# Kernel optimization log

Measured on AMD Instinct MI355X. Metric: run time of the kernel, lower is better.

Reference implementation:

```python
import jax, jax.numpy as jnp
import numpy as np

B, T, IN, H, OUT, SIM = 256, 128, 128, 1024, 256, 4
EPS_BN = 1e-5
EPS_COS = 1e-8
NEG_SLOPE = 0.2


def setup_inputs() -> dict:
    key = jax.random.key(0)
    ks = jax.random.split(key, 12)
    rn = lambda k, s: jax.random.normal(k, s, dtype=jnp.float32) * 0.05
    return {
        "x": jax.random.normal(ks[0], (B, T, IN), dtype=jnp.float32),
        "W_emb": rn(ks[1], (H, IN)),
        "b_emb": jnp.zeros((H,), jnp.float32),
        "gamma": jnp.ones((H,), jnp.float32),
        "beta": jnp.zeros((H,), jnp.float32),
        "memory": jax.random.normal(ks[2], (1, T, H), dtype=jnp.float32),
        "w_ih_x": rn(ks[3], (3 * OUT, H)),
        "w_hh_x": rn(ks[4], (3 * OUT, OUT)),
        "b_ih_x": jnp.zeros((3 * OUT,), jnp.float32),
        "b_hh_x": jnp.zeros((3 * OUT,), jnp.float32),
        "w_ih_m": rn(ks[5], (3 * OUT, H)),
        "w_hh_m": rn(ks[6], (3 * OUT, OUT)),
        "b_ih_m": jnp.zeros((3 * OUT,), jnp.float32),
        "b_hh_m": jnp.zeros((3 * OUT,), jnp.float32),
        "W_sx": rn(ks[7], (SIM, OUT)),
        "b_sx": jnp.zeros((SIM,), jnp.float32),
        "W_sm": rn(ks[8], (SIM, OUT)),
        "b_sm": jnp.zeros((SIM,), jnp.float32),
    }


def _gru(x, h, w_ih, w_hh, b_ih, b_hh):
    # PyTorch GRUCell math
    gi = x @ w_ih.T + b_ih
    gh = h @ w_hh.T + b_hh
    i_r, i_z, i_n = jnp.split(gi, 3, axis=-1)
    h_r, h_z, h_n = jnp.split(gh, 3, axis=-1)
    r = jax.nn.sigmoid(i_r + h_r)
    z = jax.nn.sigmoid(i_z + h_z)
    n = jnp.tanh(i_n + r * h_n)
    return (1.0 - z) * n + z * h


def _forward(x, W_emb, b_emb, gamma, beta, memory,
             w_ih_x, w_hh_x, b_ih_x, b_hh_x,
             w_ih_m, w_hh_m, b_ih_m, b_hh_m,
             W_sx, b_sx, W_sm, b_sm):
    # embed + LeakyReLU(0.2)
    e = x @ W_emb.T + b_emb                                  # (B,T,H)
    e = jnp.where(e >= 0, e, NEG_SLOPE * e)
    # BatchNorm1d, training mode: per-channel stats over (B,T), biased var
    mean = jnp.mean(e, axis=(0, 1))
    var = jnp.mean((e - mean) ** 2, axis=(0, 1))
    e = (e - mean) * jax.lax.rsqrt(var + EPS_BN) * gamma + beta

    mem = memory[0]                                          # (T,H) shared across batch
    b = x.shape[0]

    def step(carry, inps):
        hx, hm = carry
        xt, mt = inps                                        # (B,H), (H,)
        mtb = jnp.broadcast_to(mt, (b, mt.shape[-1]))
        hx = _gru(xt, hx, w_ih_x, w_hh_x, b_ih_x, b_hh_x)    # (B,OUT)
        hm = _gru(mtb, hm, w_ih_m, w_hh_m, b_ih_m, b_hh_m)   # (B,OUT)
        # cosine-similarity addressing between sim_size projections
        qx = hx @ W_sx.T + b_sx                              # (B,SIM)
        qm = hm @ W_sm.T + b_sm
        num = jnp.sum(qx * qm, axis=-1)
        den = (jnp.maximum(jnp.linalg.norm(qx, axis=-1), EPS_COS)
               * jnp.maximum(jnp.linalg.norm(qm, axis=-1), EPS_COS))
        g = jax.nn.sigmoid(num / den)[:, None]               # gate in (0,1)
        out = g * hx + (1.0 - g) * hm
        return (hx, hm), out

    h0 = (jnp.zeros((b, OUT), e.dtype), jnp.zeros((b, OUT), e.dtype))
    (_, _), outs = jax.lax.scan(step, h0, (e.transpose(1, 0, 2), mem))
    return outs[-1].reshape(-1, OUT)                         # out of last timestep


def reference(x, W_emb, b_emb, gamma, beta, memory,
              w_ih_x, w_hh_x, b_ih_x, b_hh_x,
              w_ih_m, w_hh_m, b_ih_m, b_hh_m,
              W_sx, b_sx, W_sm, b_sm):
    return _forward(x, W_emb, b_emb, gamma, beta, memory,
                    w_ih_x, w_hh_x, b_ih_x, b_hh_x,
                    w_ih_m, w_hh_m, b_ih_m, b_hh_m,
                    W_sx, b_sx, W_sm, b_sm)
```

## Files before the change

kernel.cpp:

```cpp
#include <hip/hip_runtime.h>
#include <stdint.h>


typedef float  f32x4 __attribute__((ext_vector_type(4)));
typedef __bf16 bf16x8 __attribute__((ext_vector_type(8)));

#define B_   256
#define T_   128
#define IN_  128
#define H_   1024
#define OUT_ 256
#define M_   32768

static constexpr size_t OFF_XB    = 0;
static constexpr size_t OFF_WEMB  = 8388608;
static constexpr size_t OFF_WHX   = 8650752;
static constexpr size_t OFF_WHM   = 9043968;
static constexpr size_t OFF_SUM   = 9437184;
static constexpr size_t OFF_SSQ   = 9441280;
static constexpr size_t OFF_FLAGS = 9445376;
static constexpr size_t OFF_BIASX = 9453568;
static constexpr size_t OFF_GIM   = 9457664;
static constexpr size_t OFF_EACT  = 9654272;
static constexpr size_t OFF_GI    = 76763136;
static constexpr size_t OFF_HXF   = 127094784;
static constexpr size_t OFF_HMF   = 127356928;
static constexpr size_t OFF_WPX   = 127373312;

__device__ __forceinline__ float sigmoidf_(float x) {
    return __builtin_amdgcn_rcpf(1.0f + __expf(-x));
}
__device__ __forceinline__ float tanhf_(float x) {
    return 1.0f - 2.0f * __builtin_amdgcn_rcpf(1.0f + __expf(2.0f * x));
}
__device__ __forceinline__ float bf16bits_(unsigned short u) {
    return __uint_as_float(((unsigned)u) << 16);
}
__device__ __forceinline__ void gload_lds16(const void* g, void* l) {
    __builtin_amdgcn_global_load_lds(
        (const __attribute__((address_space(1))) unsigned int*)g,
        (__attribute__((address_space(3))) unsigned int*)l, 16, 0, 0);
}

__global__ void prep(const float* __restrict__ x, const float* __restrict__ wemb,
                     const float* __restrict__ whx, const float* __restrict__ whm,
                     __bf16* __restrict__ xb, __bf16* __restrict__ wembb,
                     __bf16* __restrict__ whxb, __bf16* __restrict__ whmb,
                     float* __restrict__ stats , int* __restrict__ flags )
{
    long i = (long)blockIdx.x * 256 + threadIdx.x;
    if (i < 2048) stats[i] = 0.0f;
    else if (i < 2304) flags[i - 2048] = 0;
    if (i < 4194304)      xb[i] = (__bf16)x[i];
    else if (i < 4325376) wembb[i - 4194304] = (__bf16)wemb[i - 4194304];
    else if (i < 4521984) whxb[i - 4325376]  = (__bf16)whx[i - 4325376];
    else if (i < 4718592) whmb[i - 4521984]  = (__bf16)whm[i - 4521984];
}

__launch_bounds__(256)
__global__ void gemm_e(const __bf16* __restrict__ A, const __bf16* __restrict__ Bm,
                       const float* __restrict__ bias, __bf16* __restrict__ C,
                       float* __restrict__ sums, float* __restrict__ ssqs,
                       int K, int N)
{
    __shared__ __bf16 As[128 * 32];
    __shared__ __bf16 Bs[128 * 32];
    const int tid  = threadIdx.x;
    const int lane = tid & 63;
    const int wv   = tid >> 6;
    const int wm   = wv >> 1, wn = wv & 1;
    const int l15  = lane & 15, quad = lane >> 4;
    const long m0 = (long)blockIdx.x * 128;
    const long n0 = (long)blockIdx.y * 128;

    const int srow = lane >> 2;
    const int scol = (lane & 3) * 8;
    const __bf16* ag[2]; const __bf16* bg[2];
    __bf16* al[2]; __bf16* bl[2];
#pragma unroll
    for (int j = 0; j < 2; j++) {
        const int s = wv * 2 + j;
        ag[j] = A  + (m0 + s * 16 + srow) * K + scol;
        bg[j] = Bm + (n0 + s * 16 + srow) * K + scol;
        al[j] = &As[s * 512];
        bl[j] = &Bs[s * 512];
    }

    const f32x4 fz = {0.f, 0.f, 0.f, 0.f};
    f32x4 acc[4][4];
#pragma unroll
    for (int i = 0; i < 4; i++)
#pragma unroll
        for (int j = 0; j < 4; j++) acc[i][j] = fz;

    for (int k0 = 0; k0 < K; k0 += 32) {
        __syncthreads();
        gload_lds16(ag[0] + k0, al[0]);
        gload_lds16(ag[1] + k0, al[1]);
        gload_lds16(bg[0] + k0, bl[0]);
        gload_lds16(bg[1] + k0, bl[1]);
        __syncthreads();
        bf16x8 af[4], bfr[4];
#pragma unroll
        for (int mt = 0; mt < 4; mt++)
            af[mt] = *(const bf16x8*)(&As[(wm * 64 + mt * 16 + l15) * 32 + quad * 8]);
#pragma unroll
        for (int nt = 0; nt < 4; nt++)
            bfr[nt] = *(const bf16x8*)(&Bs[(wn * 64 + nt * 16 + l15) * 32 + quad * 8]);
#pragma unroll
        for (int mt = 0; mt < 4; mt++)
#pragma unroll
            for (int nt = 0; nt < 4; nt++)
                acc[mt][nt] = __builtin_amdgcn_mfma_f32_16x16x32_bf16(af[mt], bfr[nt], acc[mt][nt], 0, 0, 0);
    }

#pragma unroll
    for (int nt = 0; nt < 4; nt++) {
        const long ncol = n0 + wn * 64 + nt * 16 + l15;
        const float bi = bias[ncol];
        float s = 0.f, ss = 0.f;
#pragma unroll
        for (int mt = 0; mt < 4; mt++) {
#pragma unroll
            for (int r = 0; r < 4; r++) {
                float v = acc[mt][nt][r] + bi;
                v = (v >= 0.f) ? v : 0.2f * v;
                __bf16 hv = (__bf16)v;
                C[(m0 + wm * 64 + mt * 16 + quad * 4 + r) * (long)N + ncol] = hv;
                float fv = (float)hv; s += fv; ss += fv * fv;
            }
        }
        s += __shfl_xor(s, 16);  ss += __shfl_xor(ss, 16);
        s += __shfl_xor(s, 32);  ss += __shfl_xor(ss, 32);
        if (lane < 16) {
            atomicAdd(&sums[n0 + wn * 64 + nt * 16 + lane], s);
            atomicAdd(&ssqs[n0 + wn * 64 + nt * 16 + lane], ss);
        }
    }
}

__global__ void build_misc(const float* __restrict__ w_ih_x, const float* __restrict__ b_ih_x,
                           const float* __restrict__ b_hh_x, const float* __restrict__ sums,
                           const float* __restrict__ ssqs, const float* __restrict__ gamma,
                           const float* __restrict__ beta, __bf16* __restrict__ wpx,
                           float* __restrict__ biasx,
                           const float* __restrict__ memory, const float* __restrict__ w_ih_m,
                           const float* __restrict__ b_ih_m, const float* __restrict__ b_hh_m,
                           __bf16* __restrict__ gim)
{
    const int lane = threadIdx.x;
    if (blockIdx.x < 768) {
        const int j = blockIdx.x;
        const float inv = 1.0f / 32768.0f;
        float accv = 0.f;
#pragma unroll
        for (int i = 0; i < 16; i++) {
            int h = i * 64 + lane;
            float mean = sums[h] * inv;
            float var  = ssqs[h] * inv - mean * mean;
            float s    = rsqrtf(var + 1e-5f) * gamma[h];
            float c    = beta[h] - mean * s;
            float w = w_ih_x[(long)j * 1024 + h];
            wpx[(long)j * 1024 + h] = (__bf16)(w * s);
            accv += c * w;
        }
        for (int off = 32; off; off >>= 1) accv += __shfl_xor(accv, off);
        if (lane == 0) biasx[j] = accv + b_ih_x[j] + (j < 512 ? b_hh_x[j] : 0.0f);
    } else {
        const int g  = blockIdx.x - 768;
        const int jj = g % 768;
        const int t0 = (g / 768) * 32;
        float w[16];
#pragma unroll
        for (int i = 0; i < 16; i++) w[i] = w_ih_m[(long)jj * 1024 + i * 64 + lane];
        const float bb = b_ih_m[jj] + (jj < 512 ? b_hh_m[jj] : 0.0f);
        for (int t = t0; t < t0 + 32; t++) {
            float s = 0.f;
#pragma unroll
            for (int i = 0; i < 16; i++) s += w[i] * memory[(long)t * 1024 + i * 64 + lane];
            for (int off = 32; off; off >>= 1) s += __shfl_xor(s, off);
            if (lane == 0) gim[t * 768 + jj] = (__bf16)(s + bb);
        }
    }
}

__launch_bounds__(512, 2)
__global__ void fused(const __bf16* __restrict__ eact, const __bf16* __restrict__ wpx,
                      const float* __restrict__ biasx, __bf16* __restrict__ gi,
                      const __bf16* __restrict__ gim,
                      const __bf16* __restrict__ whx, const __bf16* __restrict__ whm,
                      const float* __restrict__ bhhx, const float* __restrict__ bhhm,
                      float* __restrict__ hxfin, float* __restrict__ hmfin,
                      int* __restrict__ flags)
{
    __shared__ union {
        struct { __bf16 hxl[2][16 * 264]; } rec;
        struct { __bf16 As[128 * 32]; __bf16 Bs[128 * 32]; } gm;
        char pad[83968];
    } sm;

    const int tid  = threadIdx.x;
    const int lane = tid & 63;
    const int v    = tid >> 6;
    const int l15  = lane & 15, quad = lane >> 4;

    if (blockIdx.x >= 17) {
        const int g  = blockIdx.x - 17;
        const int mt = g / 6;
        const long m0 = (long)mt * 128;
        const long n0 = (long)(g % 6) * 128;
        const int wm = v >> 1, wn = v & 1;

        const int srow = lane >> 2;
        const int scol = (lane & 3) * 8;
        const long m = m0 + v * 16 + srow;
        const __bf16* agA = eact + (((m & 255) << 7) + (m >> 8)) * 1024 + scol;
        const __bf16* agB = wpx + (n0 + v * 16 + srow) * 1024 + scol;
        __bf16* alA = &sm.gm.As[v * 512];
        __bf16* alB = &sm.gm.Bs[v * 512];

        const f32x4 fz = {0.f, 0.f, 0.f, 0.f};
        f32x4 acc[2][4];
#pragma unroll
        for (int i = 0; i < 2; i++)
#pragma unroll
            for (int j = 0; j < 4; j++) acc[i][j] = fz;

        for (int k0 = 0; k0 < 1024; k0 += 32) {
            __syncthreads();
            gload_lds16(agA + k0, alA);
            gload_lds16(agB + k0, alB);
            __syncthreads();
            bf16x8 af[2], bfr[4];
#pragma unroll
            for (int i = 0; i < 2; i++)
                af[i] = *(const bf16x8*)(&sm.gm.As[(wm * 32 + i * 16 + l15) * 32 + quad * 8]);
#pragma unroll
            for (int j = 0; j < 4; j++)
                bfr[j] = *(const bf16x8*)(&sm.gm.Bs[(wn * 64 + j * 16 + l15) * 32 + quad * 8]);
#pragma unroll
            for (int i = 0; i < 2; i++)
#pragma unroll
                for (int j = 0; j < 4; j++)
                    acc[i][j] = __builtin_amdgcn_mfma_f32_16x16x32_bf16(af[i], bfr[j], acc[i][j], 0, 0, 0);
        }

#pragma unroll
        for (int j = 0; j < 4; j++) {
            const long ncol = n0 + wn * 64 + j * 16 + l15;
            const float bi = biasx[ncol];
#pragma unroll
            for (int i = 0; i < 2; i++)
#pragma unroll
                for (int r = 0; r < 4; r++)
                    gi[(m0 + wm * 32 + i * 16 + quad * 4 + r) * 768 + ncol] =
                        (__bf16)(acc[i][j][r] + bi);
        }
        __syncthreads();
        if (tid == 0)
            __hip_atomic_fetch_add(&flags[mt], 1, __ATOMIC_RELEASE, __HIP_MEMORY_SCOPE_AGENT);
        return;
    }

    const int wg   = blockIdx.x;
    const bool isX = (wg < 16);
    const __bf16* wh  = isX ? whx : whm;
    const float*  bhh = isX ? bhhx : bhhm;

    bf16x8 W[6][8];
#pragma unroll
    for (int nt = 0; nt < 6; nt++) {
        const int gg = nt >> 1, ct = nt & 1;
        const long j = gg * 256 + (v * 2 + ct) * 16 + l15;
#pragma unroll
        for (int kt = 0; kt < 8; kt++)
            W[nt][kt] = *(const bf16x8*)(wh + j * 256 + kt * 32 + quad * 8);
    }
    float bhhn[2];
#pragma unroll
    for (int ct = 0; ct < 2; ct++) bhhn[ct] = bhh[512 + v * 32 + ct * 16 + l15];

    for (int i = tid; i < 16 * 264; i += 512) sm.rec.hxl[0][i] = (__bf16)0.f;

    float st[8];
#pragma unroll
    for (int i = 0; i < 8; i++) st[i] = 0.f;

    const int colb = v * 32 + l15;
    const unsigned short* gptr;
    long tstr, rstr;
    if (isX) {
        gptr = (const unsigned short*)gi + ((long)(wg * 16 + quad * 4) * 768 + colb);
        tstr = (long)256 * 768;  rstr = 768;
    } else {
        gptr = (const unsigned short*)gim + colb;
        tstr = 768;              rstr = 0;
    }
    const int myhalf = wg >> 3;

    int ready = -1;
    auto wait_tile = [&](int t) {
        if (!isX) return;
        const int need = 2 * t + myhalf;
        if (need <= ready) return;
        int probe = need + 14; if (probe > 255) probe = 255;
        if (__hip_atomic_load(&flags[probe], __ATOMIC_ACQUIRE, __HIP_MEMORY_SCOPE_AGENT) >= 6) {
            ready = probe; return;
        }
        while (__hip_atomic_load(&flags[need], __ATOMIC_ACQUIRE, __HIP_MEMORY_SCOPE_AGENT) < 6)
            __builtin_amdgcn_s_sleep(2);
        ready = need;
    };

    unsigned short gc[24], gn[24];
    auto load_g = [&](int t, unsigned short* dst) {
#pragma unroll
        for (int r = 0; r < 4; r++) {
            const unsigned short* p = gptr + (long)t * tstr + (long)r * rstr;
#pragma unroll
            for (int ct = 0; ct < 2; ct++)
#pragma unroll
                for (int g = 0; g < 3; g++)
                    dst[(r * 2 + ct) * 3 + g] = p[g * 256 + ct * 16];
        }
    };

    wait_tile(0);
    load_g(0, gc);
    __syncthreads();

    int cur = 0;
    for (int t = 0; t < 128; t++) {
        if (t < 127) { wait_tile(t + 1); load_g(t + 1, gn); }

        const f32x4 fz = {0.f, 0.f, 0.f, 0.f};
        f32x4 acc[6];
#pragma unroll
        for (int nt = 0; nt < 6; nt++) acc[nt] = fz;
        const __bf16* hxc = &sm.rec.hxl[cur][0];
#pragma unroll
        for (int kt = 0; kt < 8; kt++) {
            bf16x8 a = *(const bf16x8*)(hxc + l15 * 264 + kt * 32 + quad * 8);
#pragma unroll
            for (int nt = 0; nt < 6; nt++)
                acc[nt] = __builtin_amdgcn_mfma_f32_16x16x32_bf16(a, W[nt][kt], acc[nt], 0, 0, 0);
        }

        const int nxt = cur ^ 1;
        __bf16* hxn = &sm.rec.hxl[nxt][0];
#pragma unroll
        for (int ct = 0; ct < 2; ct++) {
            const int ob = v * 32 + ct * 16 + l15;
#pragma unroll
            for (int r = 0; r < 4; r++) {
                const int row = quad * 4 + r;
                const float gr  = bf16bits_(gc[(r * 2 + ct) * 3 + 0]);
                const float gz  = bf16bits_(gc[(r * 2 + ct) * 3 + 1]);
                const float gnv = bf16bits_(gc[(r * 2 + ct) * 3 + 2]);
                const float rg = sigmoidf_(gr + acc[ct][r]);
                const float zg = sigmoidf_(gz + acc[2 + ct][r]);
                const float ng = tanhf_(gnv + rg * (acc[4 + ct][r] + bhhn[ct]));
                float h = st[ct * 4 + r];
                h = ng + zg * (h - ng);
                st[ct * 4 + r] = h;
                hxn[row * 264 + ob] = (__bf16)h;
            }
        }
        __syncthreads();
#pragma unroll
        for (int i = 0; i < 24; i++) gc[i] = gn[i];
        cur = nxt;
    }

    float* finp = isX ? (hxfin + (long)wg * 16 * 256) : hmfin;
#pragma unroll
    for (int ct = 0; ct < 2; ct++) {
        const int ob = v * 32 + ct * 16 + l15;
#pragma unroll
        for (int r = 0; r < 4; r++)
            finp[(quad * 4 + r) * 256 + ob] = st[ct * 4 + r];
    }
}

__global__ void finalize(const float* __restrict__ hxfin, const float* __restrict__ hmfin,
                         const float* __restrict__ W_sx, const float* __restrict__ b_sx,
                         const float* __restrict__ W_sm, const float* __restrict__ b_sm,
                         float* __restrict__ out)
{
    const int b = blockIdx.x;
    const int lane = threadIdx.x;
    float qx[4], qm[4];
#pragma unroll
    for (int s = 0; s < 4; s++) {
        float px = 0.f, pm = 0.f;
#pragma unroll
        for (int i = 0; i < 4; i++) {
            int h = i * 64 + lane;
            px += W_sx[s * 256 + h] * hxfin[b * 256 + h];
            pm += W_sm[s * 256 + h] * hmfin[h];
        }
        for (int off = 32; off; off >>= 1) { px += __shfl_xor(px, off); pm += __shfl_xor(pm, off); }
        qx[s] = px + b_sx[s];
        qm[s] = pm + b_sm[s];
    }
    float num = 0.f, nx = 0.f, nm = 0.f;
#pragma unroll
    for (int s = 0; s < 4; s++) { num += qx[s] * qm[s]; nx += qx[s] * qx[s]; nm += qm[s] * qm[s]; }
    const float den = fmaxf(sqrtf(nx), 1e-8f) * fmaxf(sqrtf(nm), 1e-8f);
    const float g = 1.0f / (1.0f + __expf(-num / den));
#pragma unroll
    for (int i = 0; i < 4; i++) {
        int h = i * 64 + lane;
        out[b * 256 + h] = g * hxfin[b * 256 + h] + (1.0f - g) * hmfin[h];
    }
}

extern "C" void kernel_launch(void* const* d_in, const int* in_sizes, int n_in,
                              void* d_out, int out_size, void* d_ws, size_t ws_size,
                              hipStream_t stream)
{
    (void)in_sizes; (void)n_in; (void)out_size; (void)ws_size;
    const float* x      = (const float*)d_in[0];
    const float* W_emb  = (const float*)d_in[1];
    const float* b_emb  = (const float*)d_in[2];
    const float* gamma  = (const float*)d_in[3];
    const float* beta   = (const float*)d_in[4];
    const float* memory = (const float*)d_in[5];
    const float* w_ih_x = (const float*)d_in[6];
    const float* w_hh_x = (const float*)d_in[7];
    const float* b_ih_x = (const float*)d_in[8];
    const float* b_hh_x = (const float*)d_in[9];
    const float* w_ih_m = (const float*)d_in[10];
    const float* w_hh_m = (const float*)d_in[11];
    const float* b_ih_m = (const float*)d_in[12];
    const float* b_hh_m = (const float*)d_in[13];
    const float* W_sx   = (const float*)d_in[14];
    const float* b_sx   = (const float*)d_in[15];
    const float* W_sm   = (const float*)d_in[16];
    const float* b_sm   = (const float*)d_in[17];
    float* out = (float*)d_out;
    char* ws = (char*)d_ws;

    __bf16* xb    = (__bf16*)(ws + OFF_XB);
    __bf16* wembb = (__bf16*)(ws + OFF_WEMB);
    __bf16* whxb  = (__bf16*)(ws + OFF_WHX);
    __bf16* whmb  = (__bf16*)(ws + OFF_WHM);
    float*  sums  = (float*)(ws + OFF_SUM);
    float*  ssqs  = (float*)(ws + OFF_SSQ);
    int*    flags = (int*)(ws + OFF_FLAGS);
    float*  biasx = (float*)(ws + OFF_BIASX);
    __bf16* gim   = (__bf16*)(ws + OFF_GIM);
    __bf16* eact  = (__bf16*)(ws + OFF_EACT);
    __bf16* gi    = (__bf16*)(ws + OFF_GI);
    float*  hxf   = (float*)(ws + OFF_HXF);
    float*  hmf   = (float*)(ws + OFF_HMF);
    __bf16* wpx   = (__bf16*)(ws + OFF_WPX);

    prep<<<18432, 256, 0, stream>>>(x, W_emb, w_hh_x, w_hh_m, xb, wembb, whxb, whmb, sums, flags);
    gemm_e<<<dim3(256, 8), 256, 0, stream>>>(xb, wembb, b_emb, eact, sums, ssqs, 128, 1024);
    build_misc<<<3840, 64, 0, stream>>>(w_ih_x, b_ih_x, b_hh_x, sums, ssqs, gamma, beta, wpx, biasx,
                                        memory, w_ih_m, b_ih_m, b_hh_m, gim);
    fused<<<17 + 1536, 512, 0, stream>>>(eact, wpx, biasx, gi, gim, whxb, whmb,
                                         b_hh_x, b_hh_m, hxf, hmf, flags);
    finalize<<<256, 64, 0, stream>>>(hxf, hmf, W_sx, b_sx, W_sm, b_sm, out);
}
```

Measured before the change: 595.2 us.

## Enlarge input-projection GEMM tiles and store gates in recurrence-friendly permuted layout

```diff
diff --git a/kernel.cpp b/kernel.cpp
--- a/kernel.cpp
+++ b/kernel.cpp
@@ -4,13 +4,10 @@
 
 typedef float  f32x4 __attribute__((ext_vector_type(4)));
 typedef __bf16 bf16x8 __attribute__((ext_vector_type(8)));
+typedef unsigned short u16;
 
 #define B_   256
 #define T_   128
-#define IN_  128
-#define H_   1024
-#define OUT_ 256
-#define M_   32768
 
 static constexpr size_t OFF_XB    = 0;
 static constexpr size_t OFF_WEMB  = 8388608;
@@ -33,13 +30,20 @@
 __device__ __forceinline__ float tanhf_(float x) {
     return 1.0f - 2.0f * __builtin_amdgcn_rcpf(1.0f + __expf(2.0f * x));
 }
-__device__ __forceinline__ float bf16bits_(unsigned short u) {
+__device__ __forceinline__ float bf16bits_(u16 u) {
     return __uint_as_float(((unsigned)u) << 16);
+}
+__device__ __forceinline__ u16 f2bf_(float f) {
+    __bf16 h = (__bf16)f;
+    return __builtin_bit_cast(u16, h);
 }
 __device__ __forceinline__ void gload_lds16(const void* g, void* l) {
     __builtin_amdgcn_global_load_lds(
         (const __attribute__((address_space(1))) unsigned int*)g,
         (__attribute__((address_space(3))) unsigned int*)l, 16, 0, 0);
+}
+__device__ __forceinline__ void barrier_nodrain() {
+    __asm__ volatile("s_waitcnt lgkmcnt(0)\n\ts_barrier" ::: "memory");
 }
 
 __global__ void prep(const float* __restrict__ x, const float* __restrict__ wemb,
@@ -186,7 +190,7 @@
 
 __launch_bounds__(512, 2)
 __global__ void fused(const __bf16* __restrict__ eact, const __bf16* __restrict__ wpx,
-                      const float* __restrict__ biasx, __bf16* __restrict__ gi,
+                      const float* __restrict__ biasx, __bf16* __restrict__ gperm,
                       const __bf16* __restrict__ gim,
                       const __bf16* __restrict__ whx, const __bf16* __restrict__ whm,
                       const float* __restrict__ bhhx, const float* __restrict__ bhhm,
@@ -195,7 +199,7 @@
 {
     __shared__ union {
         struct { __bf16 hxl[2][16 * 264]; } rec;
-        struct { __bf16 As[128 * 32]; __bf16 Bs[128 * 32]; } gm;
+        struct { __bf16 As[128 * 32]; __bf16 Bs[384 * 32]; } gm;
         char pad[83968];
     } sm;
 
@@ -205,56 +209,75 @@
     const int l15  = lane & 15, quad = lane >> 4;
 
     if (blockIdx.x >= 17) {
-        const int g  = blockIdx.x - 17;
-        const int mt = g / 6;
-        const long m0 = (long)mt * 128;
-        const long n0 = (long)(g % 6) * 128;
-        const int wm = v >> 1, wn = v & 1;
-
-        const int srow = lane >> 2;
-        const int scol = (lane & 3) * 8;
-        const long m = m0 + v * 16 + srow;
-        const __bf16* agA = eact + (((m & 255) << 7) + (m >> 8)) * 1024 + scol;
-        const __bf16* agB = wpx + (n0 + v * 16 + srow) * 1024 + scol;
+        const int g   = blockIdx.x - 17;
+        const int mt  = g >> 1;
+        const int nh  = g & 1;
+        const int t   = mt >> 1, bhalf = mt & 1;
+        const int c0  = nh * 384;
+        const int mh  = v >> 2, q = v & 3;
+        const int srow = lane >> 2, scol = (lane & 3) * 8;
+
+        const __bf16* agA = eact + ((long)(bhalf * 128 + v * 16 + srow) * 128 + t) * 1024 + scol;
         __bf16* alA = &sm.gm.As[v * 512];
-        __bf16* alB = &sm.gm.Bs[v * 512];
+        const __bf16* agB[3]; __bf16* blB[3];
+#pragma unroll
+        for (int sub = 0; sub < 3; sub++) {
+            agB[sub] = wpx + (long)(c0 + v * 48 + sub * 16 + srow) * 1024 + scol;
+            blB[sub] = &sm.gm.Bs[(v * 3 + sub) * 512];
+        }
 
         const f32x4 fz = {0.f, 0.f, 0.f, 0.f};
-        f32x4 acc[2][4];
-#pragma unroll
-        for (int i = 0; i < 2; i++)
-#pragma unroll
-            for (int j = 0; j < 4; j++) acc[i][j] = fz;
+        f32x4 acc[4][6];
+#pragma unroll
+        for (int i = 0; i < 4; i++)
+#pragma unroll
+            for (int j = 0; j < 6; j++) acc[i][j] = fz;
 
         for (int k0 = 0; k0 < 1024; k0 += 32) {
             __syncthreads();
             gload_lds16(agA + k0, alA);
-            gload_lds16(agB + k0, alB);
+            gload_lds16(agB[0] + k0, blB[0]);
+            gload_lds16(agB[1] + k0, blB[1]);
+            gload_lds16(agB[2] + k0, blB[2]);
             __syncthreads();
-            bf16x8 af[2], bfr[4];
-#pragma unroll
-            for (int i = 0; i < 2; i++)
-                af[i] = *(const bf16x8*)(&sm.gm.As[(wm * 32 + i * 16 + l15) * 32 + quad * 8]);
-#pragma unroll
-            for (int j = 0; j < 4; j++)
-                bfr[j] = *(const bf16x8*)(&sm.gm.Bs[(wn * 64 + j * 16 + l15) * 32 + quad * 8]);
-#pragma unroll
-            for (int i = 0; i < 2; i++)
-#pragma unroll
-                for (int j = 0; j < 4; j++)
+            bf16x8 af[4], bfr[6];
+#pragma unroll
+            for (int i = 0; i < 4; i++)
+                af[i] = *(const bf16x8*)(&sm.gm.As[(mh * 64 + i * 16 + l15) * 32 + quad * 8]);
+#pragma unroll
+            for (int j = 0; j < 6; j++)
+                bfr[j] = *(const bf16x8*)(&sm.gm.Bs[(q * 96 + j * 16 + l15) * 32 + quad * 8]);
+#pragma unroll
+            for (int i = 0; i < 4; i++)
+#pragma unroll
+                for (int j = 0; j < 6; j++)
                     acc[i][j] = __builtin_amdgcn_mfma_f32_16x16x32_bf16(af[i], bfr[j], acc[i][j], 0, 0, 0);
         }
 
-#pragma unroll
-        for (int j = 0; j < 4; j++) {
-            const long ncol = n0 + wn * 64 + j * 16 + l15;
-            const float bi = biasx[ncol];
-#pragma unroll
-            for (int i = 0; i < 2; i++)
-#pragma unroll
-                for (int r = 0; r < 4; r++)
-                    gi[(m0 + wm * 32 + i * 16 + quad * 4 + r) * 768 + ncol] =
-                        (__bf16)(acc[i][j][r] + bi);
+        float bi[6];
+#pragma unroll
+        for (int j = 0; j < 6; j++) bi[j] = biasx[c0 + q * 96 + j * 16 + l15];
+
+        u16* gp = (u16*)gperm;
+#pragma unroll
+        for (int i = 0; i < 4; i++) {
+            const int wgi = bhalf * 8 + mh * 4 + i;
+#pragma unroll
+            for (int jp = 0; jp < 3; jp++) {
+                const int cbase = c0 + q * 96 + jp * 32;
+                const int gg = cbase >> 8;
+                const int vc = (cbase >> 5) & 7;
+                unsigned wbits[4];
+#pragma unroll
+                for (int r = 0; r < 4; r++) {
+                    u16 lo = f2bf_(acc[i][2 * jp + 0][r] + bi[2 * jp + 0]);
+                    u16 hi = f2bf_(acc[i][2 * jp + 1][r] + bi[2 * jp + 1]);
+                    wbits[r] = (unsigned)lo | ((unsigned)hi << 16);
+                }
+                uint4 o = {wbits[0], wbits[1], wbits[2], wbits[3]};
+                const long idx = (((long)t * 16 + wgi) * 8 + vc) * 1536 + (long)lane * 24 + gg * 8;
+                *(uint4*)(gp + idx) = o;
+            }
         }
         __syncthreads();
         if (tid == 0)
@@ -286,53 +309,47 @@
 #pragma unroll
     for (int i = 0; i < 8; i++) st[i] = 0.f;
 
+    const char* gpbase = (const char*)gperm + ((long)wg * 8 + v) * 3072 + (long)lane * 48;
     const int colb = v * 32 + l15;
-    const unsigned short* gptr;
-    long tstr, rstr;
-    if (isX) {
-        gptr = (const unsigned short*)gi + ((long)(wg * 16 + quad * 4) * 768 + colb);
-        tstr = (long)256 * 768;  rstr = 768;
-    } else {
-        gptr = (const unsigned short*)gim + colb;
-        tstr = 768;              rstr = 0;
-    }
     const int myhalf = wg >> 3;
 
     int ready = -1;
-    auto wait_tile = [&](int t) {
+    auto wait_tile = [&](int tt) {
         if (!isX) return;
-        const int need = 2 * t + myhalf;
+        const int need = 2 * tt + myhalf;
         if (need <= ready) return;
-        int probe = need + 14; if (probe > 255) probe = 255;
-        if (__hip_atomic_load(&flags[probe], __ATOMIC_ACQUIRE, __HIP_MEMORY_SCOPE_AGENT) >= 6) {
+        int probe = need + 28; if (probe > 255) probe = 255;
+        if (__hip_atomic_load(&flags[probe], __ATOMIC_ACQUIRE, __HIP_MEMORY_SCOPE_AGENT) >= 2) {
             ready = probe; return;
         }
-        while (__hip_atomic_load(&flags[need], __ATOMIC_ACQUIRE, __HIP_MEMORY_SCOPE_AGENT) < 6)
+        while (__hip_atomic_load(&flags[need], __ATOMIC_ACQUIRE, __HIP_MEMORY_SCOPE_AGENT) < 2)
             __builtin_amdgcn_s_sleep(2);
         ready = need;
     };
 
-    unsigned short gc[24], gn[24];
-    auto load_g = [&](int t, unsigned short* dst) {
-#pragma unroll
-        for (int r = 0; r < 4; r++) {
-            const unsigned short* p = gptr + (long)t * tstr + (long)r * rstr;
-#pragma unroll
-            for (int ct = 0; ct < 2; ct++)
-#pragma unroll
-                for (int g = 0; g < 3; g++)
-                    dst[(r * 2 + ct) * 3 + g] = p[g * 256 + ct * 16];
-        }
+    uint4 qa[3], qb[3];
+    u16   ha[6], hb[6];
+    auto load_vec = [&](int t, uint4* qd) {
+        const char* p = gpbase + (long)t * 393216;
+        qd[0] = *(const uint4*)(p);
+        qd[1] = *(const uint4*)(p + 16);
+        qd[2] = *(const uint4*)(p + 32);
     };
-
-    wait_tile(0);
-    load_g(0, gc);
+    auto load_hm = [&](int t, u16* hd) {
+        const u16* p = (const u16*)gim + (long)t * 768 + colb;
+#pragma unroll
+        for (int gg = 0; gg < 3; gg++)
+#pragma unroll
+            for (int ct = 0; ct < 2; ct++) hd[gg * 2 + ct] = p[gg * 256 + ct * 16];
+    };
+
+    wait_tile(0); wait_tile(1);
+    if (isX) { load_vec(0, qa); load_vec(1, qb); }
+    else     { load_hm(0, ha);  load_hm(1, hb);  }
     __syncthreads();
 
     int cur = 0;
-    for (int t = 0; t < 128; t++) {
-        if (t < 127) { wait_tile(t + 1); load_g(t + 1, gn); }
-
+    auto do_step = [&](const uint4* qc, const u16* hc) {
         const f32x4 fz = {0.f, 0.f, 0.f, 0.f};
         f32x4 acc[6];
 #pragma unroll
@@ -345,31 +362,54 @@
             for (int nt = 0; nt < 6; nt++)
                 acc[nt] = __builtin_amdgcn_mfma_f32_16x16x32_bf16(a, W[nt][kt], acc[nt], 0, 0, 0);
         }
-
-        const int nxt = cur ^ 1;
-        __bf16* hxn = &sm.rec.hxl[nxt][0];
+        __bf16* hxn = &sm.rec.hxl[cur ^ 1][0];
+        unsigned wr4[4], wz4[4], wn4[4];
+        if (isX) {
+            wr4[0] = qc[0].x; wr4[1] = qc[0].y; wr4[2] = qc[0].z; wr4[3] = qc[0].w;
+            wz4[0] = qc[1].x; wz4[1] = qc[1].y; wz4[2] = qc[1].z; wz4[3] = qc[1].w;
+            wn4[0] = qc[2].x; wn4[1] = qc[2].y; wn4[2] = qc[2].z; wn4[3] = qc[2].w;
+        }
 #pragma unroll
         for (int ct = 0; ct < 2; ct++) {
             const int ob = v * 32 + ct * 16 + l15;
 #pragma unroll
             for (int r = 0; r < 4; r++) {
-                const int row = quad * 4 + r;
-                const float gr  = bf16bits_(gc[(r * 2 + ct) * 3 + 0]);
-                const float gz  = bf16bits_(gc[(r * 2 + ct) * 3 + 1]);
-                const float gnv = bf16bits_(gc[(r * 2 + ct) * 3 + 2]);
+                float gr, gz, gn;
+                if (isX) {
+                    gr = __uint_as_float((ct ? (wr4[r] & 0xffff0000u) : (wr4[r] << 16)));
+                    gz = __uint_as_float((ct ? (wz4[r] & 0xffff0000u) : (wz4[r] << 16)));
+                    gn = __uint_as_float((ct ? (wn4[r] & 0xffff0000u) : (wn4[r] << 16)));
+                } else {
+                    gr = bf16bits_(hc[0 * 2 + ct]);
+                    gz = bf16bits_(hc[1 * 2 + ct]);
+                    gn = bf16bits_(hc[2 * 2 + ct]);
+                }
                 const float rg = sigmoidf_(gr + acc[ct][r]);
                 const float zg = sigmoidf_(gz + acc[2 + ct][r]);
-                const float ng = tanhf_(gnv + rg * (acc[4 + ct][r] + bhhn[ct]));
+                const float ng = tanhf_(gn + rg * (acc[4 + ct][r] + bhhn[ct]));
                 float h = st[ct * 4 + r];
                 h = ng + zg * (h - ng);
                 st[ct * 4 + r] = h;
-                hxn[row * 264 + ob] = (__bf16)h;
+                hxn[(quad * 4 + r) * 264 + ob] = (__bf16)h;
             }
         }
-        __syncthreads();
-#pragma unroll
-        for (int i = 0; i < 24; i++) gc[i] = gn[i];
-        cur = nxt;
+    };
+
+    for (int t = 0; t < 128; t += 2) {
+        do_step(qa, ha);
+        if (t + 2 < 128) {
+            wait_tile(t + 2);
+            if (isX) load_vec(t + 2, qa); else load_hm(t + 2, ha);
+        }
+        barrier_nodrain();
+        cur ^= 1;
+        do_step(qb, hb);
+        if (t + 3 < 128) {
+            wait_tile(t + 3);
+            if (isX) load_vec(t + 3, qb); else load_hm(t + 3, hb);
+        }
+        barrier_nodrain();
+        cur ^= 1;
     }
 
     float* finp = isX ? (hxfin + (long)wg * 16 * 256) : hmfin;
@@ -451,7 +491,7 @@
     float*  biasx = (float*)(ws + OFF_BIASX);
     __bf16* gim   = (__bf16*)(ws + OFF_GIM);
     __bf16* eact  = (__bf16*)(ws + OFF_EACT);
-    __bf16* gi    = (__bf16*)(ws + OFF_GI);
+    __bf16* gperm = (__bf16*)(ws + OFF_GI);
     float*  hxf   = (float*)(ws + OFF_HXF);
     float*  hmf   = (float*)(ws + OFF_HMF);
     __bf16* wpx   = (__bf16*)(ws + OFF_WPX);
@@ -460,7 +500,7 @@
     gemm_e<<<dim3(256, 8), 256, 0, stream>>>(xb, wembb, b_emb, eact, sums, ssqs, 128, 1024);
     build_misc<<<3840, 64, 0, stream>>>(w_ih_x, b_ih_x, b_hh_x, sums, ssqs, gamma, beta, wpx, biasx,
                                         memory, w_ih_m, b_ih_m, b_hh_m, gim);
-    fused<<<17 + 1536, 512, 0, stream>>>(eact, wpx, biasx, gi, gim, whxb, whmb,
-                                         b_hh_x, b_hh_m, hxf, hmf, flags);
+    fused<<<17 + 512, 512, 0, stream>>>(eact, wpx, biasx, gperm, gim, whxb, whmb,
+                                        b_hh_x, b_hh_m, hxf, hmf, flags);
     finalize<<<256, 64, 0, stream>>>(hxf, hmf, W_sx, b_sx, W_sm, b_sm, out);
 }
```

Measured after the change: 627.0 us. 1.05x slower.
